# Kernel tuning notes

Measured on AMD Instinct MI355X. Metric: run time of the kernel, lower is better.

The kernel has to match this reference:

```python
import jax, jax.numpy as jnp
import numpy as np
from jax import lax

DN = ('NCHW', 'OIHW', 'NCHW')


def _conv(x, w, groups, pad):
    return lax.conv_general_dilated(x, w, (1, 1), ((pad, pad), (pad, pad)),
                                    dimension_numbers=DN, feature_group_count=groups)


def setup_inputs() -> dict:
    key = jax.random.key(0)
    k0, k1, k2, k3, k4 = jax.random.split(key, 5)
    B, C, H, W, O = 8, 192, 56, 56, 384
    x = jax.random.normal(k0, (B, C, H, W), jnp.float32)
    # torch init: normal(0, sqrt(2/n)), n = kh*kw*out_ch
    og_dw = jax.random.normal(k1, (C, 1, 3, 3), jnp.float32) * np.sqrt(2.0 / (9 * C))
    og_pw = jax.random.normal(k2, (18, C, 1, 1), jnp.float32) * np.sqrt(2.0 / 18)
    dcn_w = jax.random.normal(k3, (C, 1, 3, 3), jnp.float32) * np.sqrt(2.0 / (9 * C))
    pw_w = jax.random.normal(k4, (O, C, 1, 1), jnp.float32) * np.sqrt(2.0 / O)
    return {'x': x, 'og_dw': og_dw, 'og_pw': og_pw, 'dcn_w': dcn_w, 'pw_w': pw_w}


def _deform_sample(x, dy, dx):
    # x: [B,C,H,W]; dy,dx: [B,9,H,W] learned offsets. Returns [B,C,9,H,W]
    B, C, H, W = x.shape
    ky = (jnp.repeat(jnp.arange(3), 3) - 1).astype(x.dtype)   # tap row offsets
    kx = (jnp.tile(jnp.arange(3), 3) - 1).astype(x.dtype)     # tap col offsets
    gh = jnp.arange(H, dtype=x.dtype)[:, None]
    gw = jnp.arange(W, dtype=x.dtype)[None, :]
    ys = gh[None, None] + ky[None, :, None, None] + dy        # [B,9,H,W]
    xs = gw[None, None] + kx[None, :, None, None] + dx
    y0 = jnp.floor(ys)
    x0 = jnp.floor(xs)
    ty = ys - y0
    tx = xs - x0
    y0i = y0.astype(jnp.int32)
    x0i = x0.astype(jnp.int32)
    xf = x.reshape(B, C, H * W)
    gather = jax.vmap(lambda xb, ib: xb[:, ib])  # ([C,HW],[9,H,W]) -> [C,9,H,W]
    val = jnp.zeros((B, C, 9, H, W), x.dtype)
    corners = [(y0i, x0i, (1 - ty) * (1 - tx)),
               (y0i, x0i + 1, (1 - ty) * tx),
               (y0i + 1, x0i, ty * (1 - tx)),
               (y0i + 1, x0i + 1, ty * tx)]
    for yi, xi, wgt in corners:
        valid = ((yi >= 0) & (yi < H) & (xi >= 0) & (xi < W)).astype(x.dtype)
        idx = jnp.clip(yi, 0, H - 1) * W + jnp.clip(xi, 0, W - 1)  # [B,9,H,W]
        v = gather(xf, idx)                                        # [B,C,9,H,W]
        val = val + v * (wgt * valid)[:, None]
    return val


def reference(x, og_dw, og_pw, dcn_w, pw_w):
    B, C, H, W = x.shape
    O = pw_w.shape[0]
    # offset generator: depthwise 3x3 then 1x1 -> 18 channels, clamped
    off = _conv(_conv(x, og_dw, C, 1), og_pw, 1, 0)
    off = jnp.clip(off, -1.0, 1.0)
    off = off.reshape(B, 9, 2, H, W)
    dy, dx = off[:, :, 0], off[:, :, 1]
    # depthwise deformable conv 3x3
    val = _deform_sample(x, dy, dx)                       # [B,C,9,H,W]
    y = jnp.einsum('bckhw,ck->bchw', val, dcn_w.reshape(C, 9))
    # pointwise conv + Hardswish
    y = jnp.einsum('bchw,oc->bohw', y, pw_w.reshape(O, C))
    return y * jnp.clip(y + 3.0, 0.0, 6.0) / 6.0
```

## Files before the change

### kernel.cpp

```cpp
#include <hip/hip_runtime.h>
#include <hip/hip_fp16.h>

#define TPB 256
constexpr int B_ = 8, C_ = 192, H_ = 56, W_ = 56, O_ = 384;
constexpr int HW_ = H_ * W_;
constexpr int NOFF = 18;
constexpr int NPIX = B_ * HW_;
constexpr int K2 = 9 * C_;

typedef __attribute__((ext_vector_type(8))) short short8v;
typedef __attribute__((ext_vector_type(4))) float f32x4;
typedef __attribute__((ext_vector_type(2))) float f32x2;

__device__ inline unsigned short f2bf(float f) {
  unsigned u = __builtin_bit_cast(unsigned, f);
  unsigned r = (u + 0x7fffu + ((u >> 16) & 1u)) >> 16;
  return (unsigned short)r;
}
__device__ inline float bflo(unsigned u) {
  return __builtin_bit_cast(float, u << 16);
}
__device__ inline float bfhi(unsigned u) {
  return __builtin_bit_cast(float, u & 0xffff0000u);
}

__global__ __launch_bounds__(TPB) void k_xtp(const float* __restrict__ x,
                                             const float* __restrict__ og_dw,
                                             const float* __restrict__ og_pw,
                                             const float* __restrict__ pw,
                                             const float* __restrict__ dcn,
                                             unsigned short* __restrict__ xt,
                                             unsigned short* __restrict__ wtb,
                                             unsigned short* __restrict__ w2b,
                                             float* __restrict__ dcnT_g) {
  __shared__ unsigned short tile[64 * 198];
  int tid = threadIdx.x;
  int P0 = blockIdx.x * 64;
  int b = blockIdx.y;

  int gid = (blockIdx.y * 49 + blockIdx.x) * TPB + tid;
#pragma unroll
  for (int it = 0; it < 2; ++it) {
    int i = gid + it * (49 * 8 * TPB);
    if (i < O_ * C_) {
      wtb[i] = f2bf(pw[i]);
    } else if (i < O_ * C_ + 32 * K2) {
      int j = i - O_ * C_;
      int o = j / K2, k = j - o * K2;
      int tap = k / C_, c = k - tap * C_;
      float v = 0.f;
      if (o < NOFF) v = og_pw[o * C_ + c] * og_dw[c * 9 + tap];
      w2b[j] = f2bf(v);
    } else if (i < O_ * C_ + 32 * K2 + 9 * C_) {
      int j2 = i - O_ * C_ - 32 * K2;
      int k = j2 / C_, c = j2 - k * C_;
      dcnT_g[j2] = dcn[c * 9 + k];
    }
  }

#pragma unroll
  for (int i = 0; i < 48; ++i) {
    int idx = i * TPB + tid;
    int px = idx & 63;
    int c = idx >> 6;
    float v = x[((size_t)(b * C_ + c)) * HW_ + P0 + px];
    tile[px * 198 + c] = f2bf(v);
  }
  __syncthreads();
  unsigned* xtu = (unsigned*)xt;
#pragma unroll
  for (int i = 0; i < 24; ++i) {
    int d = i * TPB + tid;
    int px = d / 96;
    int c2 = d - px * 96;
    unsigned v = *(const unsigned*)&tile[px * 198 + c2 * 2];
    xtu[((size_t)b * HW_ + P0 + px) * 96 + c2] = v;
  }
}

__global__ __launch_bounds__(TPB) void k_off2s(const unsigned short* __restrict__ xt,
                                               const unsigned short* __restrict__ w2b,
                                               float* __restrict__ offp3) {
  __shared__ __align__(16) unsigned short hal[80 * 192];
  int tid = threadIdx.x;
  int w0 = blockIdx.x * 8;
  int h0 = blockIdx.y * 8;
  int bz = blockIdx.z;
  int b = bz & 7;
  int s = bz >> 3;
  int dy = s - 1;

  char* sb = (char*)hal;
  const uint4* xu4 = (const uint4*)xt;
#pragma unroll
  for (int i = 0; i < 8; ++i) {
    int u = i * TPB + tid;
    if (u < 1920) {
      int pos = u / 24, c4 = u - pos * 24;
      int ry = pos / 10;
      int gy = h0 + ry + dy;
      int gx = w0 - 1 + (pos - ry * 10);
      uint4 v = {0u, 0u, 0u, 0u};
      if ((unsigned)gy < (unsigned)H_ && (unsigned)gx < (unsigned)W_)
        v = xu4[((size_t)b * HW_ + gy * W_ + gx) * 24 + c4];
      *(uint4*)(sb + pos * 384 + ((c4 * 16) ^ ((pos & 7) << 4))) = v;
    }
  }
  __syncthreads();

  int wid = tid >> 6;
  int lane = tid & 63;
  int col = lane & 15;
  int kg = lane >> 4;
  int gpx = wid * 16 + col;
  int py = gpx >> 3, px_ = gpx & 7;

  f32x4 acc0 = (f32x4){0.f, 0.f, 0.f, 0.f};
  f32x4 acc1 = (f32x4){0.f, 0.f, 0.f, 0.f};

#pragma unroll
  for (int j = 0; j < 3; ++j) {
    int tap = 3 * s + j;
    int pos = py * 10 + px_ + j;
    int pbase = pos * 384;
    int psw = (pos & 7) << 4;
    const unsigned short* wrow = w2b + tap * C_ + kg * 8;
#pragma unroll
    for (int cs = 0; cs < 6; ++cs) {
      short8v bfrag = *(const short8v*)(sb + pbase + ((cs * 64 + kg * 16) ^ psw));
      short8v a0 = *(const short8v*)(wrow + cs * 32 + (size_t)col * K2);
      short8v a1 = *(const short8v*)(wrow + cs * 32 + (size_t)(16 + col) * K2);
      acc0 = __builtin_amdgcn_mfma_f32_16x16x32_bf16(a0, bfrag, acc0, 0, 0, 0);
      acc1 = __builtin_amdgcn_mfma_f32_16x16x32_bf16(a1, bfrag, acc1, 0, 0, 0);
    }
  }

  float* ob = offp3 + (size_t)(s * B_ + b) * NOFF * HW_ + (h0 + py) * W_ + w0 + px_;
#pragma unroll
  for (int reg = 0; reg < 4; ++reg) {
    int o0 = kg * 4 + reg;
    ob[(size_t)o0 * HW_] = acc0[reg];
    int o1 = 16 + kg * 4 + reg;
    if (o1 < NOFF) ob[(size_t)o1 * HW_] = acc1[reg];
  }
}

__global__ __launch_bounds__(512, 4) void k_deform11(const unsigned short* __restrict__ xt,
                                                     const float* __restrict__ offp3,
                                                     const float* __restrict__ dcnT_g,
                                                     unsigned short* __restrict__ y1t) {
  __shared__ __align__(16) unsigned short hal[117 * 192];
  __shared__ __align__(16) f32x4 w4tab[288];
  __shared__ int postab[288];
  int tid = threadIdx.x;
  int bid = blockIdx.x;
  int b = bid & 7;
  int tile = bid >> 3;
  int ty = tile / 7;
  int h0 = ty * 4;
  int w0 = (tile - ty * 7) * 8;

  uint4* halu4 = (uint4*)hal;
  const uint4* xu4 = (const uint4*)xt;
#pragma unroll
  for (int i = 0; i < 6; ++i) {
    int u = i * 512 + tid;
    if (u < 2808) {
      int pos = u / 24;
      int ly = pos / 13, lx = pos - ly * 13;
      int gy = h0 - 2 + ly, gx = w0 - 2 + lx;
      uint4 v = {0u, 0u, 0u, 0u};
      if ((unsigned)gy < (unsigned)H_ && (unsigned)gx < (unsigned)W_)
        v = xu4[((size_t)b * HW_ + gy * W_ + gx) * 24 + (u - pos * 24)];
      halu4[u] = v;
    }
  }

  if (tid < 288) {
    int pxl = tid / 9, tap = tid - pxl * 9;
    int py = pxl >> 3, pxx = pxl & 7;
    int h = h0 + py, w = w0 + pxx;
    int hw = h * W_ + w;
    const float* p0 = offp3 + (size_t)b * NOFF * HW_ + hw;
    const float* p1 = p0 + (size_t)B_ * NOFF * HW_;
    const float* p2 = p1 + (size_t)B_ * NOFF * HW_;
    int t3 = tap / 3;
    int ky = t3 - 1, kx = tap - t3 * 3 - 1;
    size_t ody = (size_t)(2 * tap) * HW_;
    size_t odx = ody + HW_;
    float dyv = p0[ody] + p1[ody] + p2[ody];
    float dxv = p0[odx] + p1[odx] + p2[odx];
    dyv = fminf(fmaxf(dyv, -1.f), 1.f);
    dxv = fminf(fmaxf(dxv, -1.f), 1.f);
    float ys = (float)(h + ky) + dyv;
    float xs = (float)(w + kx) + dxv;
    float y0f = floorf(ys), x0f = floorf(xs);
    float tyf = ys - y0f, txf = xs - x0f;
    int y0 = (int)y0f, x0 = (int)x0f;
    float fy0 = ((unsigned)y0 < (unsigned)H_) ? 1.f : 0.f;
    float fy1 = ((unsigned)(y0 + 1) < (unsigned)H_) ? 1.f : 0.f;
    float fx0 = ((unsigned)x0 < (unsigned)W_) ? 1.f : 0.f;
    float fx1 = ((unsigned)(x0 + 1) < (unsigned)W_) ? 1.f : 0.f;
    float omty = 1.f - tyf, omtx = 1.f - txf;
    f32x4 w4;
    w4.x = omty * omtx * fy0 * fx0;
    w4.y = omty * txf * fy0 * fx1;
    w4.z = tyf * omtx * fy1 * fx0;
    w4.w = tyf * txf * fy1 * fx1;
    w4tab[tid] = w4;
    postab[tid] = (y0 - (h0 - 2)) * 13 + (x0 - (w0 - 2));
  }
  __syncthreads();

  int pl = tid >> 4;
  int lg = tid & 15;
  int py = pl >> 3, pxx = pl & 7;
  int hw = (h0 + py) * W_ + w0 + pxx;
  int co0 = lg * 4;

  f32x2 acc2[6];
#pragma unroll
  for (int j = 0; j < 6; ++j) acc2[j] = (f32x2){0.f, 0.f};

#pragma unroll
  for (int tap = 0; tap < 9; ++tap) {
    f32x4 w4 = w4tab[pl * 9 + tap];
    int posA = postab[pl * 9 + tap];
    const unsigned short* base = hal + posA * 192 + co0;
#pragma unroll
    for (int rep = 0; rep < 3; ++rep) {
      int co = rep * 64;
      uint2 u00 = *(const uint2*)(base + co);
      uint2 u01 = *(const uint2*)(base + 192 + co);
      uint2 u10 = *(const uint2*)(base + 13 * 192 + co);
      uint2 u11 = *(const uint2*)(base + 14 * 192 + co);
      f32x4 dw = *(const f32x4*)&dcnT_g[tap * C_ + co0 + co];
      f32x2 v00l = (f32x2){bflo(u00.x), bfhi(u00.x)};
      f32x2 v01l = (f32x2){bflo(u01.x), bfhi(u01.x)};
      f32x2 v10l = (f32x2){bflo(u10.x), bfhi(u10.x)};
      f32x2 v11l = (f32x2){bflo(u11.x), bfhi(u11.x)};
      f32x2 v00h = (f32x2){bflo(u00.y), bfhi(u00.y)};
      f32x2 v01h = (f32x2){bflo(u01.y), bfhi(u01.y)};
      f32x2 v10h = (f32x2){bflo(u10.y), bfhi(u10.y)};
      f32x2 v11h = (f32x2){bflo(u11.y), bfhi(u11.y)};
      f32x2 sl = v00l * w4.x + v01l * w4.y + v10l * w4.z + v11l * w4.w;
      f32x2 sh = v00h * w4.x + v01h * w4.y + v10h * w4.z + v11h * w4.w;
      acc2[rep * 2 + 0] += sl * (f32x2){dw.x, dw.y};
      acc2[rep * 2 + 1] += sh * (f32x2){dw.z, dw.w};
    }
  }

  size_t ob = ((size_t)b * HW_ + hw) * C_ + co0;
#pragma unroll
  for (int rep = 0; rep < 3; ++rep) {
    uint2 pk;
    pk.x = (unsigned)f2bf(acc2[rep * 2][0]) | ((unsigned)f2bf(acc2[rep * 2][1]) << 16);
    pk.y = (unsigned)f2bf(acc2[rep * 2 + 1][0]) | ((unsigned)f2bf(acc2[rep * 2 + 1][1]) << 16);
    *(uint2*)(y1t + ob + rep * 64) = pk;
  }
}

__global__ __launch_bounds__(TPB) void k_gemm5(const unsigned short* __restrict__ y1t,
                                               const unsigned short* __restrict__ wtb,
                                               float* __restrict__ out) {
  __shared__ __align__(16) unsigned short bsm[64 * 192];
  int tid = threadIdx.x;
  int bid = blockIdx.x;
  int b = bid & 7;
  int r = bid >> 3;
  int mhalf = r / 49;
  int tile = r - mhalf * 49;
  int n0 = b * HW_ + tile * 64;
  int mbase = mhalf * 192;

  const uint4* src = (const uint4*)(y1t + (size_t)n0 * C_);
  char* sbase = (char*)bsm;
#pragma unroll
  for (int i = 0; i < 6; ++i) {
    int u = i * TPB + tid;
    int row = u / 24;
    int c4 = u - row * 24;
    uint4 v = src[u];
    *(uint4*)(sbase + row * 384 + ((c4 * 16) ^ ((row & 7) << 4))) = v;
  }
  __syncthreads();

  int wid = tid >> 6;
  int lane = tid & 63;
  int col = lane & 15;
  int kg = lane >> 4;
  int wr = wid >> 1;
  int wc = wid & 1;

#pragma unroll 1
  for (int mi = 0; mi < 3; ++mi) {
    int m0 = mbase + mi * 64;
    f32x4 acc[2][2];
#pragma unroll
    for (int mf = 0; mf < 2; ++mf)
#pragma unroll
      for (int nf = 0; nf < 2; ++nf) acc[mf][nf] = (f32x4){0.f, 0.f, 0.f, 0.f};

#pragma unroll
    for (int k0 = 0; k0 < C_; k0 += 32) {
      short8v a[2], bfr[2];
#pragma unroll
      for (int mf = 0; mf < 2; ++mf)
        a[mf] = *(const short8v*)(wtb + (m0 + wr * 32 + mf * 16 + col) * C_ + k0 + kg * 8);
#pragma unroll
      for (int nf = 0; nf < 2; ++nf) {
        int brow = wc * 32 + nf * 16 + col;
        int kb = (k0 + kg * 8) * 2;
        bfr[nf] = *(const short8v*)(sbase + brow * 384 + (kb ^ ((brow & 7) << 4)));
      }
#pragma unroll
      for (int mf = 0; mf < 2; ++mf)
#pragma unroll
        for (int nf = 0; nf < 2; ++nf)
          acc[mf][nf] = __builtin_amdgcn_mfma_f32_16x16x32_bf16(a[mf], bfr[nf], acc[mf][nf], 0, 0, 0);
    }

#pragma unroll
    for (int mf = 0; mf < 2; ++mf) {
#pragma unroll
      for (int nf = 0; nf < 2; ++nf) {
        int p = n0 + wc * 32 + nf * 16 + col;
        int hw = p - b * HW_;
#pragma unroll
        for (int reg = 0; reg < 4; ++reg) {
          int o = m0 + wr * 32 + mf * 16 + kg * 4 + reg;
          float a = acc[mf][nf][reg];
          float rr = a * fminf(fmaxf(a + 3.f, 0.f), 6.f) * (1.f / 6.f);
          out[((size_t)b * O_ + o) * HW_ + hw] = rr;
        }
      }
    }
  }
}

extern "C" void kernel_launch(void* const* d_in, const int* in_sizes, int n_in,
                              void* d_out, int out_size, void* d_ws, size_t ws_size,
                              hipStream_t stream) {
  const float* x = (const float*)d_in[0];
  const float* og_dw = (const float*)d_in[1];
  const float* og_pw = (const float*)d_in[2];
  const float* dcn_w = (const float*)d_in[3];
  const float* pw_w = (const float*)d_in[4];
  float* out = (float*)d_out;

  float* ws = (float*)d_ws;
  float* offp3 = ws;
  float* dcnT_g = offp3 + 3 * (size_t)B_ * NOFF * HW_;
  unsigned short* y1t = (unsigned short*)(dcnT_g + 9 * C_);
  unsigned short* wtb = y1t + (size_t)NPIX * C_;
  unsigned short* x_t = wtb + (size_t)O_ * C_;
  unsigned short* w2b = x_t + (size_t)NPIX * C_;

  k_xtp<<<dim3(HW_ / 64, B_), TPB, 0, stream>>>(x, og_dw, og_pw, pw_w, dcn_w,
                                                x_t, wtb, w2b, dcnT_g);
  k_off2s<<<dim3(W_ / 8, H_ / 8, B_ * 3), TPB, 0, stream>>>(x_t, w2b, offp3);
  k_deform11<<<196 * 4 * B_ / 8, 512, 0, stream>>>(x_t, offp3, dcnT_g, y1t);
  k_gemm5<<<NPIX / 64 * 2, TPB, 0, stream>>>(y1t, wtb, out);
}
```

Baseline: 79.73 us.

## Fuse deformable sampling with pointwise GEMM via shared-memory tile

Merges the deformable depthwise kernel and the pointwise bf16 GEMM into one kernel. Each 32-pixel block writes its deformed channel vector to a swizzled shared tile, then its 8 waves compute all 384 output channels with MFMA and apply Hardswish. This drops the y1t global round-trip and one kernel launch. In exchange, every block re-reads the full 384x192 weight matrix from global or L2 for only 32 pixels, and the GEMM tile is narrow (N=32), which lowers MFMA reuse.

Result: faster. 77.30 us (-3.1%).

```diff
diff --git a/kernel.cpp b/kernel.cpp
--- a/kernel.cpp
+++ b/kernel.cpp
@@ -145,13 +145,15 @@
   }
 }
 
-__global__ __launch_bounds__(512, 4) void k_deform11(const unsigned short* __restrict__ xt,
-                                                     const float* __restrict__ offp3,
-                                                     const float* __restrict__ dcnT_g,
-                                                     unsigned short* __restrict__ y1t) {
+__global__ __launch_bounds__(512, 4) void k_dfgemm(const unsigned short* __restrict__ xt,
+                                                   const float* __restrict__ offp3,
+                                                   const float* __restrict__ dcnT_g,
+                                                   const unsigned short* __restrict__ wtb,
+                                                   float* __restrict__ out) {
   __shared__ __align__(16) unsigned short hal[117 * 192];
   __shared__ __align__(16) f32x4 w4tab[288];
   __shared__ int postab[288];
+  __shared__ __align__(16) unsigned short bsm[32 * 192];
   int tid = threadIdx.x;
   int bid = blockIdx.x;
   int b = bid & 7;
@@ -212,126 +214,91 @@
   }
   __syncthreads();
 
-  int pl = tid >> 4;
-  int lg = tid & 15;
-  int py = pl >> 3, pxx = pl & 7;
-  int hw = (h0 + py) * W_ + w0 + pxx;
-  int co0 = lg * 4;
-
-  f32x2 acc2[6];
-#pragma unroll
-  for (int j = 0; j < 6; ++j) acc2[j] = (f32x2){0.f, 0.f};
-
-#pragma unroll
-  for (int tap = 0; tap < 9; ++tap) {
-    f32x4 w4 = w4tab[pl * 9 + tap];
-    int posA = postab[pl * 9 + tap];
-    const unsigned short* base = hal + posA * 192 + co0;
+  {
+    int pl = tid >> 4;
+    int lg = tid & 15;
+    int co0 = lg * 4;
+
+    f32x2 acc2[6];
+#pragma unroll
+    for (int j = 0; j < 6; ++j) acc2[j] = (f32x2){0.f, 0.f};
+
+#pragma unroll
+    for (int tap = 0; tap < 9; ++tap) {
+      f32x4 w4 = w4tab[pl * 9 + tap];
+      int posA = postab[pl * 9 + tap];
+      const unsigned short* base = hal + posA * 192 + co0;
+#pragma unroll
+      for (int rep = 0; rep < 3; ++rep) {
+        int co = rep * 64;
+        uint2 u00 = *(const uint2*)(base + co);
+        uint2 u01 = *(const uint2*)(base + 192 + co);
+        uint2 u10 = *(const uint2*)(base + 13 * 192 + co);
+        uint2 u11 = *(const uint2*)(base + 14 * 192 + co);
+        f32x4 dw = *(const f32x4*)&dcnT_g[tap * C_ + co0 + co];
+        f32x2 v00l = (f32x2){bflo(u00.x), bfhi(u00.x)};
+        f32x2 v01l = (f32x2){bflo(u01.x), bfhi(u01.x)};
+        f32x2 v10l = (f32x2){bflo(u10.x), bfhi(u10.x)};
+        f32x2 v11l = (f32x2){bflo(u11.x), bfhi(u11.x)};
+        f32x2 v00h = (f32x2){bflo(u00.y), bfhi(u00.y)};
+        f32x2 v01h = (f32x2){bflo(u01.y), bfhi(u01.y)};
+        f32x2 v10h = (f32x2){bflo(u10.y), bfhi(u10.y)};
+        f32x2 v11h = (f32x2){bflo(u11.y), bfhi(u11.y)};
+        f32x2 sl = v00l * w4.x + v01l * w4.y + v10l * w4.z + v11l * w4.w;
+        f32x2 sh = v00h * w4.x + v01h * w4.y + v10h * w4.z + v11h * w4.w;
+        acc2[rep * 2 + 0] += sl * (f32x2){dw.x, dw.y};
+        acc2[rep * 2 + 1] += sh * (f32x2){dw.z, dw.w};
+      }
+    }
+
+    char* sbase = (char*)bsm;
+    int psw = (pl & 7) << 4;
 #pragma unroll
     for (int rep = 0; rep < 3; ++rep) {
-      int co = rep * 64;
-      uint2 u00 = *(const uint2*)(base + co);
-      uint2 u01 = *(const uint2*)(base + 192 + co);
-      uint2 u10 = *(const uint2*)(base + 13 * 192 + co);
-      uint2 u11 = *(const uint2*)(base + 14 * 192 + co);
-      f32x4 dw = *(const f32x4*)&dcnT_g[tap * C_ + co0 + co];
-      f32x2 v00l = (f32x2){bflo(u00.x), bfhi(u00.x)};
-      f32x2 v01l = (f32x2){bflo(u01.x), bfhi(u01.x)};
-      f32x2 v10l = (f32x2){bflo(u10.x), bfhi(u10.x)};
-      f32x2 v11l = (f32x2){bflo(u11.x), bfhi(u11.x)};
-      f32x2 v00h = (f32x2){bflo(u00.y), bfhi(u00.y)};
-      f32x2 v01h = (f32x2){bflo(u01.y), bfhi(u01.y)};
-      f32x2 v10h = (f32x2){bflo(u10.y), bfhi(u10.y)};
-      f32x2 v11h = (f32x2){bflo(u11.y), bfhi(u11.y)};
-      f32x2 sl = v00l * w4.x + v01l * w4.y + v10l * w4.z + v11l * w4.w;
-      f32x2 sh = v00h * w4.x + v01h * w4.y + v10h * w4.z + v11h * w4.w;
-      acc2[rep * 2 + 0] += sl * (f32x2){dw.x, dw.y};
-      acc2[rep * 2 + 1] += sh * (f32x2){dw.z, dw.w};
-    }
-  }
-
-  size_t ob = ((size_t)b * HW_ + hw) * C_ + co0;
-#pragma unroll
-  for (int rep = 0; rep < 3; ++rep) {
-    uint2 pk;
-    pk.x = (unsigned)f2bf(acc2[rep * 2][0]) | ((unsigned)f2bf(acc2[rep * 2][1]) << 16);
-    pk.y = (unsigned)f2bf(acc2[rep * 2 + 1][0]) | ((unsigned)f2bf(acc2[rep * 2 + 1][1]) << 16);
-    *(uint2*)(y1t + ob + rep * 64) = pk;
-  }
-}
-
-__global__ __launch_bounds__(TPB) void k_gemm5(const unsigned short* __restrict__ y1t,
-                                               const unsigned short* __restrict__ wtb,
-                                               float* __restrict__ out) {
-  __shared__ __align__(16) unsigned short bsm[64 * 192];
-  int tid = threadIdx.x;
-  int bid = blockIdx.x;
-  int b = bid & 7;
-  int r = bid >> 3;
-  int mhalf = r / 49;
-  int tile = r - mhalf * 49;
-  int n0 = b * HW_ + tile * 64;
-  int mbase = mhalf * 192;
-
-  const uint4* src = (const uint4*)(y1t + (size_t)n0 * C_);
-  char* sbase = (char*)bsm;
-#pragma unroll
-  for (int i = 0; i < 6; ++i) {
-    int u = i * TPB + tid;
-    int row = u / 24;
-    int c4 = u - row * 24;
-    uint4 v = src[u];
-    *(uint4*)(sbase + row * 384 + ((c4 * 16) ^ ((row & 7) << 4))) = v;
+      uint2 pk;
+      pk.x = (unsigned)f2bf(acc2[rep * 2][0]) | ((unsigned)f2bf(acc2[rep * 2][1]) << 16);
+      pk.y = (unsigned)f2bf(acc2[rep * 2 + 1][0]) | ((unsigned)f2bf(acc2[rep * 2 + 1][1]) << 16);
+      *(uint2*)(sbase + pl * 384 + ((lg * 8 + rep * 128) ^ psw)) = pk;
+    }
   }
   __syncthreads();
 
-  int wid = tid >> 6;
-  int lane = tid & 63;
-  int col = lane & 15;
-  int kg = lane >> 4;
-  int wr = wid >> 1;
-  int wc = wid & 1;
+  {
+    const char* sbase = (const char*)bsm;
+    int wid = tid >> 6;
+    int lane = tid & 63;
+    int col = lane & 15;
+    int kg = lane >> 4;
 
 #pragma unroll 1
-  for (int mi = 0; mi < 3; ++mi) {
-    int m0 = mbase + mi * 64;
-    f32x4 acc[2][2];
-#pragma unroll
-    for (int mf = 0; mf < 2; ++mf)
-#pragma unroll
-      for (int nf = 0; nf < 2; ++nf) acc[mf][nf] = (f32x4){0.f, 0.f, 0.f, 0.f};
-
-#pragma unroll
-    for (int k0 = 0; k0 < C_; k0 += 32) {
-      short8v a[2], bfr[2];
-#pragma unroll
-      for (int mf = 0; mf < 2; ++mf)
-        a[mf] = *(const short8v*)(wtb + (m0 + wr * 32 + mf * 16 + col) * C_ + k0 + kg * 8);
+    for (int mi = 0; mi < 3; ++mi) {
+      int m0 = (wid * 3 + mi) * 16;
+      f32x4 acc[2];
+      acc[0] = (f32x4){0.f, 0.f, 0.f, 0.f};
+      acc[1] = (f32x4){0.f, 0.f, 0.f, 0.f};
+
+#pragma unroll
+      for (int k0 = 0; k0 < C_; k0 += 32) {
+        short8v a = *(const short8v*)(wtb + (size_t)(m0 + col) * C_ + k0 + kg * 8);
+#pragma unroll
+        for (int nf = 0; nf < 2; ++nf) {
+          int brow = nf * 16 + col;
+          int kb = (k0 + kg * 8) * 2;
+          short8v bfr = *(const short8v*)(sbase + brow * 384 + (kb ^ ((brow & 7) << 4)));
+          acc[nf] = __builtin_amdgcn_mfma_f32_16x16x32_bf16(a, bfr, acc[nf], 0, 0, 0);
+        }
+      }
+
 #pragma unroll
       for (int nf = 0; nf < 2; ++nf) {
-        int brow = wc * 32 + nf * 16 + col;
-        int kb = (k0 + kg * 8) * 2;
-        bfr[nf] = *(const short8v*)(sbase + brow * 384 + (kb ^ ((brow & 7) << 4)));
-      }
-#pragma unroll
-      for (int mf = 0; mf < 2; ++mf)
-#pragma unroll
-        for (int nf = 0; nf < 2; ++nf)
-          acc[mf][nf] = __builtin_amdgcn_mfma_f32_16x16x32_bf16(a[mf], bfr[nf], acc[mf][nf], 0, 0, 0);
-    }
-
-#pragma unroll
-    for (int mf = 0; mf < 2; ++mf) {
-#pragma unroll
-      for (int nf = 0; nf < 2; ++nf) {
-        int p = n0 + wc * 32 + nf * 16 + col;
-        int hw = p - b * HW_;
+        int px = nf * 16 + col;
+        int hw = (h0 + (px >> 3)) * W_ + w0 + (px & 7);
 #pragma unroll
         for (int reg = 0; reg < 4; ++reg) {
-          int o = m0 + wr * 32 + mf * 16 + kg * 4 + reg;
-          float a = acc[mf][nf][reg];
-          float rr = a * fminf(fmaxf(a + 3.f, 0.f), 6.f) * (1.f / 6.f);
-          out[((size_t)b * O_ + o) * HW_ + hw] = rr;
+          int o = m0 + kg * 4 + reg;
+          float a = acc[nf][reg];
+          float r = a * fminf(fmaxf(a + 3.f, 0.f), 6.f) * (1.f / 6.f);
+          out[((size_t)b * O_ + o) * HW_ + hw] = r;
         }
       }
     }
@@ -351,14 +318,12 @@
   float* ws = (float*)d_ws;
   float* offp3 = ws;
   float* dcnT_g = offp3 + 3 * (size_t)B_ * NOFF * HW_;
-  unsigned short* y1t = (unsigned short*)(dcnT_g + 9 * C_);
-  unsigned short* wtb = y1t + (size_t)NPIX * C_;
+  unsigned short* wtb = (unsigned short*)(dcnT_g + 9 * C_);
   unsigned short* x_t = wtb + (size_t)O_ * C_;
   unsigned short* w2b = x_t + (size_t)NPIX * C_;
 
   k_xtp<<<dim3(HW_ / 64, B_), TPB, 0, stream>>>(x, og_dw, og_pw, pw_w, dcn_w,
                                                 x_t, wtb, w2b, dcnT_g);
   k_off2s<<<dim3(W_ / 8, H_ / 8, B_ * 3), TPB, 0, stream>>>(x_t, w2b, offp3);
-  k_deform11<<<196 * 4 * B_ / 8, 512, 0, stream>>>(x_t, offp3, dcnT_g, y1t);
-  k_gemm5<<<NPIX / 64 * 2, TPB, 0, stream>>>(y1t, wtb, out);
-}
+  k_dfgemm<<<196 * 4 * B_ / 8, 512, 0, stream>>>(x_t, offp3, dcnT_g, wtb, out);
+}
```
